# Kernel optimization log

Hardware: AMD Instinct MI355X
Metric: run time of the kernel (lower is better)

The kernel has to match this reference:

```python
import jax, jax.numpy as jnp
import numpy as np

B, E, L, H = 4, 1024, 2048, 16
DH = E // H
SCALE = E ** -0.5  # note: original scales by embedding_dim**-0.5, not head_dim**-0.5


def setup_inputs() -> dict:
    key = jax.random.key(0)
    k1, k2, k3 = jax.random.split(key, 3)
    x = jax.random.normal(k1, (B, E, L), dtype=jnp.float32)
    # Linear init: randn(d_in, d_out) / d_in
    W_qkv = jax.random.normal(k2, (E, E), dtype=jnp.float32) / E
    W_proj = jax.random.normal(k3, (E, E), dtype=jnp.float32) / E
    b_proj = jnp.zeros((E,), dtype=jnp.float32)
    return {"x": x, "W_qkv": W_qkv, "W_proj": W_proj, "b_proj": b_proj}


def reference(x, W_qkv, W_proj, b_proj):
    b, e, l = x.shape
    # shared Q=K=V projection (channels-first Linear: (x^T @ M)^T)
    kqv = jnp.einsum('bel,ef->bfl', x, W_qkv)            # [B, E, L]
    kqv = kqv.reshape(b, H, DH, l)                        # [B, H, Dh, L]
    # scores[b,h,i,j] = <kqv[...,i], kqv[...,j]> over head dim
    scores = jnp.einsum('bhdi,bhdj->bhij', kqv, kqv)      # [B, H, L, L]
    # mask strictly-lower triangle (i > j), then scale; softmax over query axis (-2)
    mask = jnp.tril(jnp.ones((l, l), dtype=bool), k=-1)
    scores = jnp.where(mask, -jnp.inf, scores * SCALE)
    att = jax.nn.softmax(scores, axis=-2)                 # normalize over i (rows)
    # t[...,d,j] = sum_i kqv[...,d,i] * att[...,i,j]
    t = jnp.einsum('bhdi,bhij->bhdj', kqv, att).reshape(b, e, l)
    # output projection with bias (dropout is identity in eval)
    out = jnp.einsum('bel,ef->bfl', t, W_proj) + b_proj[None, :, None]
    return out
```

## Files before the change

### kernel.cpp

```cpp
#include <hip/hip_runtime.h>
#include <stdint.h>
#include <math.h>

#define B_ 4
#define E_ 1024
#define L_ 2048
#define H_ 16
#define DH_ 64
#define SCALE_ 0.03125f

typedef __bf16 bf16;
typedef __bf16 bf16x8 __attribute__((ext_vector_type(8)));
typedef __bf16 bf16x4 __attribute__((ext_vector_type(4)));
typedef float f32x4 __attribute__((ext_vector_type(4)));

__device__ __forceinline__ f32x4 mfma16(bf16x8 a, bf16x8 b, f32x4 c) {
  return __builtin_amdgcn_mfma_f32_16x16x32_bf16(a, b, c, 0, 0, 0);
}

__device__ __forceinline__ void gl_lds16(const void* g, void* lds) {
  auto* lp = reinterpret_cast<__attribute__((address_space(3))) unsigned int*>(
      reinterpret_cast<uintptr_t>(lds));
  const auto* gp = reinterpret_cast<const __attribute__((address_space(1))) unsigned int*>(
      reinterpret_cast<uintptr_t>(g));
  __builtin_amdgcn_global_load_lds(gp, lp, 16, 0, 0);
}

__global__ __launch_bounds__(256) void tconv(const float* __restrict__ in,
                                             bf16* __restrict__ out, int R, int C) {
  in  += (size_t)blockIdx.z * R * C;
  out += (size_t)blockIdx.z * R * C;
  __shared__ float t[32][33];
  const int r0 = blockIdx.x * 32, c0 = blockIdx.y * 32;
  const int lx = threadIdx.x & 31, ly = threadIdx.x >> 5;
#pragma unroll
  for (int q = 0; q < 4; q++)
    t[ly + q * 8][lx] = in[(size_t)(r0 + ly + q * 8) * C + c0 + lx];
  __syncthreads();
#pragma unroll
  for (int q = 0; q < 4; q++) {
    int c = ly + q * 8;
    out[(size_t)(c0 + c) * R + r0 + lx] = (bf16)t[lx][c];
  }
}

__global__ __launch_bounds__(256) void wconv(const float* __restrict__ in0,
                                             const float* __restrict__ in1,
                                             bf16* __restrict__ out0,
                                             bf16* __restrict__ out1) {
  const float* in = blockIdx.z ? in1 : in0;
  bf16* out = blockIdx.z ? out1 : out0;
  __shared__ float t[32][33];
  const int r0 = blockIdx.x * 32, c0 = blockIdx.y * 32;
  const int lx = threadIdx.x & 31, ly = threadIdx.x >> 5;
#pragma unroll
  for (int q = 0; q < 4; q++)
    t[ly + q * 8][lx] = in[(size_t)(r0 + ly + q * 8) * E_ + c0 + lx];
  __syncthreads();
#pragma unroll
  for (int q = 0; q < 4; q++) {
    int c = ly + q * 8;
    out[(size_t)(c0 + c) * E_ + r0 + lx] = (bf16)t[lx][c];
  }
}

template <int EPI>
__global__ __launch_bounds__(256) void gemm_bt(const bf16* __restrict__ A,
                                               const bf16* __restrict__ Bt,
                                               bf16* __restrict__ outT,
                                               bf16* __restrict__ outD,
                                               float* __restrict__ outF,
                                               const float* __restrict__ bias) {
  constexpr int M = E_, N = L_, K = E_;
  constexpr int NIT = K / 32;
  const int bm = blockIdx.x, bn = blockIdx.y, b = blockIdx.z;
  __shared__ bf16 As[2][128 * 32];
  __shared__ bf16 Bs[2][128 * 32];
  const int tid = threadIdx.x, w = tid >> 6, l = tid & 63;
  const int wm = (w >> 1) << 6, wn = (w & 1) << 6;
  const bf16* Ap = A + (size_t)bm * 128 * K;
  const bf16* Bp = Bt + (size_t)b * N * K + (size_t)bn * 128 * K;
  f32x4 acc[4][4] = {};
  const int g0 = (w * 2 + 0) * 64 + l, g1 = (w * 2 + 1) * 64 + l;
  const int r0 = g0 >> 2, s0 = (g0 & 3) ^ ((r0 >> 1) & 3);
  const int r1 = g1 >> 2, s1 = (g1 & 3) ^ ((r1 >> 1) & 3);

#define STAGE_G(kt_, buf)                                              \
  do {                                                                 \
    gl_lds16(Ap + (size_t)r0 * K + (kt_) + s0 * 8, &As[buf][g0 * 8]);  \
    gl_lds16(Ap + (size_t)r1 * K + (kt_) + s1 * 8, &As[buf][g1 * 8]);  \
    gl_lds16(Bp + (size_t)r0 * K + (kt_) + s0 * 8, &Bs[buf][g0 * 8]);  \
    gl_lds16(Bp + (size_t)r1 * K + (kt_) + s1 * 8, &Bs[buf][g1 * 8]);  \
  } while (0)

  STAGE_G(0, 0);
  asm volatile("s_waitcnt vmcnt(0)" ::: "memory");
  __syncthreads();
#pragma unroll 1
  for (int it = 0; it < NIT; it++) {
    const int cur = it & 1;
    if (it + 1 < NIT) STAGE_G((it + 1) * 32, cur ^ 1);
    bf16x8 af[4], bfr[4];
#pragma unroll
    for (int fm = 0; fm < 4; fm++) {
      int row = wm + fm * 16 + (l & 15);
      int gg = row * 4 + ((l >> 4) ^ ((row >> 1) & 3));
      af[fm] = *(const bf16x8*)(&As[cur][gg * 8]);
    }
#pragma unroll
    for (int fn = 0; fn < 4; fn++) {
      int row = wn + fn * 16 + (l & 15);
      int gg = row * 4 + ((l >> 4) ^ ((row >> 1) & 3));
      bfr[fn] = *(const bf16x8*)(&Bs[cur][gg * 8]);
    }
#pragma unroll
    for (int fm = 0; fm < 4; fm++)
#pragma unroll
      for (int fn = 0; fn < 4; fn++)
        acc[fm][fn] = mfma16(af[fm], bfr[fn], acc[fm][fn]);
    asm volatile("s_waitcnt vmcnt(0)" ::: "memory");
    __syncthreads();
  }
#undef STAGE_G
  const int cm = bm * 128 + wm, cn = bn * 128 + wn;
  if (EPI == 0) {
#pragma unroll
    for (int fn = 0; fn < 4; fn++) {
#pragma unroll
      for (int fm = 0; fm < 4; fm++) {
        int n = cn + fn * 16 + (l & 15);
        int m = cm + fm * 16 + ((l >> 4) << 2);
        f32x4 v = acc[fm][fn];
        bf16x4 pv = {(bf16)v[0], (bf16)v[1], (bf16)v[2], (bf16)v[3]};
        *(bf16x4*)(outT + (size_t)b * N * M + (size_t)n * M + m) = pv;
#pragma unroll
        for (int r = 0; r < 4; r++)
          outD[(size_t)b * M * N + (size_t)(m + r) * N + n] = pv[r];
      }
    }
  } else {
#pragma unroll
    for (int fm = 0; fm < 4; fm++) {
      int m = cm + fm * 16 + ((l >> 4) << 2);
#pragma unroll
      for (int r = 0; r < 4; r++) {
        float bv = bias[m + r];
#pragma unroll
        for (int fn = 0; fn < 4; fn++) {
          int n = cn + fn * 16 + (l & 15);
          outF[(size_t)b * M * N + (size_t)(m + r) * N + n] = acc[fm][fn][r] + bv;
        }
      }
    }
  }
}

__global__ __launch_bounds__(512) void attn(const bf16* __restrict__ kqvT,
                                            const bf16* __restrict__ kqvD,
                                            bf16* __restrict__ tT) {
  const int linear = (int)blockIdx.x + 16 * ((int)blockIdx.y + 16 * (int)blockIdx.z);
  const int qb = 15 - (linear >> 6);
  const int h = linear & 15, b = (linear >> 4) & 3;
  const int tid = threadIdx.x, w = tid >> 6, l = tid & 63;
  const int j0 = qb * 128 + w * 16;
  __shared__ bf16 Ks[2][64 * 64];
  __shared__ bf16 Vs[2][64 * 64];
  __shared__ bf16 Ps[8][16 * 64];
  const size_t bT = (size_t)b * L_ * E_;
  const size_t bD = (size_t)b * E_ * L_;
  bf16x8 qa[2];
  {
    size_t qoff = bT + (size_t)(j0 + (l & 15)) * E_ + h * 64 + ((l >> 4) << 3);
    qa[0] = *(const bf16x8*)(kqvT + qoff);
    qa[1] = *(const bf16x8*)(kqvT + qoff + 32);
#pragma unroll
    for (int e = 0; e < 8; e++) {
      qa[0][e] = (bf16)((float)qa[0][e] * SCALE_);
      qa[1][e] = (bf16)((float)qa[1][e] * SCALE_);
    }
  }
  float mrun[4] = {0.f, 0.f, 0.f, 0.f};
  float lsum[4] = {0.f, 0.f, 0.f, 0.f};
  f32x4 tacc[4] = {};
  bf16* myPs = &Ps[w][0];
  const int g = w * 64 + l;
  const int rS = g >> 3, sS = (g & 7) ^ (rS & 7);
  const int nch = 2 * (qb + 1);

#define STAGE(c, buf)                                                                  \
  do {                                                                                 \
    const int i0_ = (c) * 64;                                                          \
    gl_lds16(kqvT + bT + (size_t)(i0_ + rS) * E_ + h * 64 + sS * 8, &Ks[buf][g * 8]);  \
    gl_lds16(kqvD + bD + (size_t)(h * 64 + rS) * L_ + i0_ + sS * 8, &Vs[buf][g * 8]);  \
  } while (0)

  STAGE(0, 0);
  asm volatile("s_waitcnt vmcnt(0)" ::: "memory");
  __syncthreads();

#pragma unroll 1
  for (int c = 0; c < nch; c++) {
    const int cur = c & 1;
    if (c + 1 < nch) STAGE(c + 1, cur ^ 1);
    const int i0 = c * 64;
    const bf16* Kc = &Ks[cur][0];
    const bf16* Vc = &Vs[cur][0];
    if (i0 <= j0 + 15) {
      f32x4 sacc[4];
      __builtin_amdgcn_s_setprio(1);
#pragma unroll
      for (int fi = 0; fi < 4; fi++) {
        int row = fi * 16 + (l & 15);
        bf16x8 k0 = *(const bf16x8*)(Kc + row * 64 + (((l >> 4) ^ (row & 7)) << 3));
        bf16x8 k1 = *(const bf16x8*)(Kc + row * 64 + ((((l >> 4) + 4) ^ (row & 7)) << 3));
        f32x4 z = {};
        z = mfma16(qa[0], k0, z);
        z = mfma16(qa[1], k1, z);
        sacc[fi] = z;
      }
      __builtin_amdgcn_s_setprio(0);
      const int jrb = j0 + ((l >> 4) << 2);
      if (i0 + 63 > j0) {
#pragma unroll
        for (int fi = 0; fi < 4; fi++) {
          int i = i0 + fi * 16 + (l & 15);
#pragma unroll
          for (int r = 0; r < 4; r++)
            if (i > jrb + r) sacc[fi][r] = -INFINITY;
        }
      }
      bool ov = false;
#pragma unroll
      for (int fi = 0; fi < 4; fi++)
#pragma unroll
        for (int r = 0; r < 4; r++) ov |= (sacc[fi][r] > mrun[r] + 8.f);
      if (__any(ov)) {
        float mx[4];
#pragma unroll
        for (int r = 0; r < 4; r++)
          mx[r] = fmaxf(fmaxf(sacc[0][r], sacc[1][r]), fmaxf(sacc[2][r], sacc[3][r]));
#pragma unroll
        for (int r = 0; r < 4; r++) {
          mx[r] = fmaxf(mx[r], __shfl_xor(mx[r], 1));
          mx[r] = fmaxf(mx[r], __shfl_xor(mx[r], 2));
          mx[r] = fmaxf(mx[r], __shfl_xor(mx[r], 4));
          mx[r] = fmaxf(mx[r], __shfl_xor(mx[r], 8));
        }
#pragma unroll
        for (int r = 0; r < 4; r++) {
          float mn = fmaxf(mrun[r], mx[r]);
          float a = __expf(mrun[r] - mn);
          lsum[r] *= a;
#pragma unroll
          for (int fd = 0; fd < 4; fd++) tacc[fd][r] *= a;
          mrun[r] = mn;
        }
      }
#pragma unroll
      for (int fi = 0; fi < 4; fi++) {
        int icol = fi * 16 + (l & 15);
#pragma unroll
        for (int r = 0; r < 4; r++) {
          float p = __expf(sacc[fi][r] - mrun[r]);
          lsum[r] += p;
          int jl = ((l >> 4) << 2) + r;
          int slot = (icol >> 3) ^ (jl & 7);
          myPs[jl * 64 + slot * 8 + (icol & 7)] = (bf16)p;
        }
      }
      bf16x8 pa[2];
      {
        int jl = l & 15;
#pragma unroll
        for (int kc = 0; kc < 2; kc++)
          pa[kc] = *(const bf16x8*)(myPs + jl * 64 + (((kc * 4 + (l >> 4)) ^ (jl & 7)) << 3));
      }
      __builtin_amdgcn_s_setprio(1);
#pragma unroll
      for (int fd = 0; fd < 4; fd++) {
        int row = fd * 16 + (l & 15);
#pragma unroll
        for (int kc = 0; kc < 2; kc++) {
          bf16x8 vf = *(const bf16x8*)(Vc + row * 64 + (((kc * 4 + (l >> 4)) ^ (row & 7)) << 3));
          tacc[fd] = mfma16(pa[kc], vf, tacc[fd]);
        }
      }
      __builtin_amdgcn_s_setprio(0);
    }
    asm volatile("s_waitcnt vmcnt(0)" ::: "memory");
    __syncthreads();
  }
#undef STAGE
#pragma unroll
  for (int r = 0; r < 4; r++) {
    lsum[r] += __shfl_xor(lsum[r], 1);
    lsum[r] += __shfl_xor(lsum[r], 2);
    lsum[r] += __shfl_xor(lsum[r], 4);
    lsum[r] += __shfl_xor(lsum[r], 8);
  }
#pragma unroll
  for (int r = 0; r < 4; r++) {
    int j = j0 + ((l >> 4) << 2) + r;
    float inv = 1.0f / lsum[r];
#pragma unroll
    for (int fd = 0; fd < 4; fd++) {
      int d = fd * 16 + (l & 15);
      tT[bT + (size_t)j * E_ + h * 64 + d] = (bf16)(tacc[fd][r] * inv);
    }
  }
}

extern "C" void kernel_launch(void* const* d_in, const int* in_sizes, int n_in,
                              void* d_out, int out_size, void* d_ws, size_t ws_size,
                              hipStream_t stream) {
  const float* x     = (const float*)d_in[0];
  const float* Wqkv  = (const float*)d_in[1];
  const float* Wproj = (const float*)d_in[2];
  const float* bias  = (const float*)d_in[3];
  float* out = (float*)d_out;
  char* ws = (char*)d_ws;
  bf16* Wt_qkv  = (bf16*)ws;
  bf16* Wt_proj = (bf16*)(ws + (2ull << 20));
  bf16* xT      = (bf16*)(ws + (4ull << 20));
  bf16* kqvT    = (bf16*)(ws + (20ull << 20));
  bf16* kqvD    = (bf16*)(ws + (36ull << 20));
  bf16* tT      = xT;

  wconv<<<dim3(32, 32, 2), 256, 0, stream>>>(Wqkv, Wproj, Wt_qkv, Wt_proj);
  tconv<<<dim3(32, 64, B_), 256, 0, stream>>>(x, xT, E_, L_);
  gemm_bt<0><<<dim3(8, 16, B_), 256, 0, stream>>>(Wt_qkv, xT, kqvT, kqvD,
                                                  (float*)nullptr, (const float*)nullptr);
  attn<<<dim3(16, 16, B_), 512, 0, stream>>>(kqvT, kqvD, tT);
  gemm_bt<1><<<dim3(8, 16, B_), 256, 0, stream>>>(Wt_proj, tT, (bf16*)nullptr,
                                                  (bf16*)nullptr, out, bias);
}
```

Before: 213.0 us.

## Shrink GEMM tile to 128x64, single-buffer LDS, swizzle block order across XCDs

The projection GEMMs now use 128x64 output tiles instead of 128x128, which doubles the block count to 1024 and roughly halves per-block LDS and accumulator registers. The double-buffered prefetch is replaced with a single shared buffer that is loaded, waited on and synced every k-step. A linear block index is remapped so consecutive blocks go to different XCDs. The aim is more blocks in flight and better occupancy, but the change gives up the overlap of global loads with MFMA work and raises B-operand traffic per output.

```diff
diff --git a/kernel.cpp b/kernel.cpp
--- a/kernel.cpp
+++ b/kernel.cpp
@@ -72,60 +72,50 @@
                                                float* __restrict__ outF,
                                                const float* __restrict__ bias) {
   constexpr int M = E_, N = L_, K = E_;
-  constexpr int NIT = K / 32;
-  const int bm = blockIdx.x, bn = blockIdx.y, b = blockIdx.z;
-  __shared__ bf16 As[2][128 * 32];
-  __shared__ bf16 Bs[2][128 * 32];
+  const int lin = (int)blockIdx.x;
+  const int lgc = (lin & 7) * 128 + (lin >> 3);
+  const int bn = lgc & 31, bm = (lgc >> 5) & 7, b = lgc >> 8;
+  __shared__ bf16 AB[192 * 32];
   const int tid = threadIdx.x, w = tid >> 6, l = tid & 63;
-  const int wm = (w >> 1) << 6, wn = (w & 1) << 6;
+  const int wm = (w >> 1) << 6, wn = (w & 1) << 5;
   const bf16* Ap = A + (size_t)bm * 128 * K;
-  const bf16* Bp = Bt + (size_t)b * N * K + (size_t)bn * 128 * K;
-  f32x4 acc[4][4] = {};
-  const int g0 = (w * 2 + 0) * 64 + l, g1 = (w * 2 + 1) * 64 + l;
+  const bf16* Bp = Bt + (size_t)b * N * K + (size_t)bn * 64 * K;
+  f32x4 acc[4][2] = {};
+  const int g0 = tid, g1 = tid + 256, g2 = tid + 512;
   const int r0 = g0 >> 2, s0 = (g0 & 3) ^ ((r0 >> 1) & 3);
   const int r1 = g1 >> 2, s1 = (g1 & 3) ^ ((r1 >> 1) & 3);
-
-#define STAGE_G(kt_, buf)                                              \
-  do {                                                                 \
-    gl_lds16(Ap + (size_t)r0 * K + (kt_) + s0 * 8, &As[buf][g0 * 8]);  \
-    gl_lds16(Ap + (size_t)r1 * K + (kt_) + s1 * 8, &As[buf][g1 * 8]);  \
-    gl_lds16(Bp + (size_t)r0 * K + (kt_) + s0 * 8, &Bs[buf][g0 * 8]);  \
-    gl_lds16(Bp + (size_t)r1 * K + (kt_) + s1 * 8, &Bs[buf][g1 * 8]);  \
-  } while (0)
-
-  STAGE_G(0, 0);
-  asm volatile("s_waitcnt vmcnt(0)" ::: "memory");
-  __syncthreads();
+  const int r2 = g2 >> 2, s2 = (g2 & 3) ^ ((r2 >> 1) & 3);
 #pragma unroll 1
-  for (int it = 0; it < NIT; it++) {
-    const int cur = it & 1;
-    if (it + 1 < NIT) STAGE_G((it + 1) * 32, cur ^ 1);
-    bf16x8 af[4], bfr[4];
+  for (int kt = 0; kt < K; kt += 32) {
+    __syncthreads();
+    gl_lds16(Ap + (size_t)r0 * K + kt + s0 * 8, AB + g0 * 8);
+    gl_lds16(Ap + (size_t)r1 * K + kt + s1 * 8, AB + g1 * 8);
+    gl_lds16(Bp + (size_t)(r2 - 128) * K + kt + s2 * 8, AB + g2 * 8);
+    asm volatile("s_waitcnt vmcnt(0)" ::: "memory");
+    __syncthreads();
+    bf16x8 af[4], bfr[2];
 #pragma unroll
     for (int fm = 0; fm < 4; fm++) {
       int row = wm + fm * 16 + (l & 15);
       int gg = row * 4 + ((l >> 4) ^ ((row >> 1) & 3));
-      af[fm] = *(const bf16x8*)(&As[cur][gg * 8]);
-    }
-#pragma unroll
-    for (int fn = 0; fn < 4; fn++) {
-      int row = wn + fn * 16 + (l & 15);
+      af[fm] = *(const bf16x8*)(AB + gg * 8);
+    }
+#pragma unroll
+    for (int fn = 0; fn < 2; fn++) {
+      int row = 128 + wn + fn * 16 + (l & 15);
       int gg = row * 4 + ((l >> 4) ^ ((row >> 1) & 3));
-      bfr[fn] = *(const bf16x8*)(&Bs[cur][gg * 8]);
+      bfr[fn] = *(const bf16x8*)(AB + gg * 8);
     }
 #pragma unroll
     for (int fm = 0; fm < 4; fm++)
 #pragma unroll
-      for (int fn = 0; fn < 4; fn++)
+      for (int fn = 0; fn < 2; fn++)
         acc[fm][fn] = mfma16(af[fm], bfr[fn], acc[fm][fn]);
-    asm volatile("s_waitcnt vmcnt(0)" ::: "memory");
-    __syncthreads();
-  }
-#undef STAGE_G
-  const int cm = bm * 128 + wm, cn = bn * 128 + wn;
+  }
+  const int cm = bm * 128 + wm, cn = bn * 64 + wn;
   if (EPI == 0) {
 #pragma unroll
-    for (int fn = 0; fn < 4; fn++) {
+    for (int fn = 0; fn < 2; fn++) {
 #pragma unroll
       for (int fm = 0; fm < 4; fm++) {
         int n = cn + fn * 16 + (l & 15);
@@ -146,7 +136,7 @@
       for (int r = 0; r < 4; r++) {
         float bv = bias[m + r];
 #pragma unroll
-        for (int fn = 0; fn < 4; fn++) {
+        for (int fn = 0; fn < 2; fn++) {
           int n = cn + fn * 16 + (l & 15);
           outF[(size_t)b * M * N + (size_t)(m + r) * N + n] = acc[fm][fn][r] + bv;
         }
@@ -328,9 +318,9 @@
 
   wconv<<<dim3(32, 32, 2), 256, 0, stream>>>(Wqkv, Wproj, Wt_qkv, Wt_proj);
   tconv<<<dim3(32, 64, B_), 256, 0, stream>>>(x, xT, E_, L_);
-  gemm_bt<0><<<dim3(8, 16, B_), 256, 0, stream>>>(Wt_qkv, xT, kqvT, kqvD,
-                                                  (float*)nullptr, (const float*)nullptr);
+  gemm_bt<0><<<dim3(1024, 1, 1), 256, 0, stream>>>(Wt_qkv, xT, kqvT, kqvD,
+                                                   (float*)nullptr, (const float*)nullptr);
   attn<<<dim3(16, 16, B_), 512, 0, stream>>>(kqvT, kqvD, tT);
-  gemm_bt<1><<<dim3(8, 16, B_), 256, 0, stream>>>(Wt_proj, tT, (bf16*)nullptr,
-                                                  (bf16*)nullptr, out, bias);
-}
+  gemm_bt<1><<<dim3(1024, 1, 1), 256, 0, stream>>>(Wt_proj, tT, (bf16*)nullptr,
+                                                   (bf16*)nullptr, out, bias);
+}
```

After: 214.5 us. Within noise of the previous version (+0.7%).
